# Kernel optimization log

Hardware: AMD Instinct MI355X
Metric: run time of the kernel (lower is better)

The kernel has to match this reference:

```python
import jax, jax.numpy as jnp
import numpy as np

N_USER, N_FOOD, N_ING, N_CAT, N_HAB = 50000, 50000, 50000, 5000, 5000
N_NODES = N_USER + N_FOOD + N_ING + N_CAT + N_HAB  # 160000
E = 600000
R = 8
D = 128  # common_dim == hidden_dim


def _linear(x, W, b):
    # W: (in, out)
    return x @ W + b


def _rgcn_conv(x, src, dst, edge_type, W, root, bias):
    """PyG RGCNConv with aggr='mean': out = x@root + bias + sum_r mean_{r-edges into i}(W_r x_j)."""
    n = x.shape[0]
    out = x @ root + bias
    for r in range(R):  # static small loop over relations
        mask = (edge_type == r)
        h_r = x @ W[r]                          # (N, O)
        msg = h_r[src] * mask[:, None].astype(x.dtype)  # (E, O)
        s = jax.ops.segment_sum(msg, dst, num_segments=n)
        cnt = jax.ops.segment_sum(mask.astype(x.dtype), dst, num_segments=n)
        out = out + s / jnp.maximum(cnt, 1.0)[:, None]
    return out


def setup_inputs() -> dict:
    key = jax.random.key(0)
    ks = jax.random.split(key, 32)
    s = 0.05
    inp = {
        'x_user': jax.random.normal(ks[0], (N_USER, 256), jnp.float32),
        'x_food': jax.random.normal(ks[1], (N_FOOD, 128), jnp.float32),
        'x_ingredient': jax.random.normal(ks[2], (N_ING, 128), jnp.float32),
        'x_category': jax.random.normal(ks[3], (N_CAT, 64), jnp.float32),
        'x_habit': jax.random.normal(ks[4], (N_HAB, 64), jnp.float32),
        'edge_index': jax.random.randint(ks[5], (2, E), 0, N_NODES, jnp.int32),
        'edge_type': jax.random.randint(ks[6], (E,), 0, R, jnp.int32),
        # init linears (in, out)
        'Wu': jax.random.normal(ks[7], (256, D), jnp.float32) * s,
        'bu': jnp.zeros((D,), jnp.float32),
        'Wf': jax.random.normal(ks[8], (128, D), jnp.float32) * s,
        'bf': jnp.zeros((D,), jnp.float32),
        'Wi': jax.random.normal(ks[9], (128, D), jnp.float32) * s,
        'bi': jnp.zeros((D,), jnp.float32),
        'Wc': jax.random.normal(ks[10], (64, D), jnp.float32) * s,
        'bc': jnp.zeros((D,), jnp.float32),
        'Wh': jax.random.normal(ks[11], (64, D), jnp.float32) * s,
        'bh': jnp.zeros((D,), jnp.float32),
        # conv1
        'W1': jax.random.normal(ks[12], (R, D, D), jnp.float32) * s,
        'root1': jax.random.normal(ks[13], (D, D), jnp.float32) * s,
        'bias1': jnp.zeros((D,), jnp.float32),
        # conv2
        'W2': jax.random.normal(ks[14], (R, D, D), jnp.float32) * s,
        'root2': jax.random.normal(ks[15], (D, D), jnp.float32) * s,
        'bias2': jnp.zeros((D,), jnp.float32),
    }
    return inp


def reference(x_user, x_food, x_ingredient, x_category, x_habit,
              edge_index, edge_type,
              Wu, bu, Wf, bf, Wi, bi, Wc, bc, Wh, bh,
              W1, root1, bias1, W2, root2, bias2):
    # per-type input projections then concat in fixed order
    x_all = jnp.concatenate([
        _linear(x_user, Wu, bu),
        _linear(x_food, Wf, bf),
        _linear(x_ingredient, Wi, bi),
        _linear(x_category, Wc, bc),
        _linear(x_habit, Wh, bh),
    ], axis=0)  # (N_NODES, D)
    src, dst = edge_index[0], edge_index[1]
    x = _rgcn_conv(x_all, src, dst, edge_type, W1, root1, bias1)
    x = jax.nn.relu(x)
    # dropout is identity in eval mode
    x = _rgcn_conv(x, src, dst, edge_type, W2, root2, bias2)
    return x
```

## Files before the change

kernel.cpp:

```cpp
#include <hip/hip_runtime.h>

typedef unsigned short ushort_t;
typedef unsigned int uint_t;
typedef __attribute__((ext_vector_type(8))) __bf16 bf16x8;
typedef __attribute__((ext_vector_type(4))) float f32x4;
typedef __attribute__((ext_vector_type(4))) uint_t uint4v;

#define NN 160000
#define DD 128
#define EE 600000
#define RR 8
#define NRR (NN * RR)
#define CAP1 486000
#define WTOT 376832

__device__ __forceinline__ ushort_t f2b(float f) {
  uint_t u = __float_as_uint(f);
  u = u + 0x7fffu + ((u >> 16) & 1u);
  return (ushort_t)(u >> 16);
}
__device__ __forceinline__ float b2f(ushort_t u) {
  return __uint_as_float(((uint_t)u) << 16);
}

struct WSrcs { const float* s[9]; };

__global__ void wconv_all_kernel(WSrcs srcs, ushort_t* __restrict__ wbuf) {
  int i = blockIdx.x * blockDim.x + threadIdx.x;
  if (i >= WTOT) return;
  int m, start, K;
  if      (i < 32768)  { m = 0; start = 0;      K = 256; }
  else if (i < 49152)  { m = 1; start = 32768;  K = 128; }
  else if (i < 65536)  { m = 2; start = 49152;  K = 128; }
  else if (i < 73728)  { m = 3; start = 65536;  K = 64;  }
  else if (i < 81920)  { m = 4; start = 73728;  K = 64;  }
  else if (i < 98304)  { m = 5; start = 81920;  K = 128; }
  else if (i < 114688) { m = 6; start = 98304;  K = 128; }
  else if (i < 245760) { m = 7; start = 114688; K = 128; }
  else                 { m = 8; start = 245760; K = 128; }
  int local = i - start;
  int per = K * 128;
  int mat = local / per, rem = local - mat * per;
  int k = rem >> 7, n = rem & 127;
  wbuf[start + mat * per + n * K + k] = f2b(srcs.s[m][local]);
}

__global__ __launch_bounds__(256, 2) void gemm_proj(
    const float* __restrict__ Ain, const ushort_t* __restrict__ WT,
    const float* __restrict__ bias, ushort_t* __restrict__ Cout, int M, int K) {
  __shared__ ushort_t As[128 * 128];
  __shared__ ushort_t Ws[128 * 128];
  const int tid = threadIdx.x;
  const int bm = blockIdx.x * 128;
  const int wave = tid >> 6, lane = tid & 63;
  const int lr = lane & 15;
  const int lg = lane >> 4;

  f32x4 acc[2][8];
#pragma unroll
  for (int mt = 0; mt < 2; ++mt)
#pragma unroll
    for (int nt = 0; nt < 8; ++nt) acc[mt][nt] = {0.f, 0.f, 0.f, 0.f};

  for (int k0 = 0; k0 < K; k0 += 128) {
#pragma unroll
    for (int it = 0; it < 8; ++it) {
      int row = it * 16 + (tid >> 4);
      int c = tid & 15;
      uint4v val = {0, 0, 0, 0};
      int grow = bm + row, gk = k0 + c * 8;
      if (grow < M && gk < K) {
        const float* ap = Ain + (size_t)grow * K + gk;
        float4 v0 = *(const float4*)ap;
        float4 v1 = *(const float4*)(ap + 4);
        val[0] = (uint_t)f2b(v0.x) | ((uint_t)f2b(v0.y) << 16);
        val[1] = (uint_t)f2b(v0.z) | ((uint_t)f2b(v0.w) << 16);
        val[2] = (uint_t)f2b(v1.x) | ((uint_t)f2b(v1.y) << 16);
        val[3] = (uint_t)f2b(v1.z) | ((uint_t)f2b(v1.w) << 16);
      }
      *(uint4v*)&As[row * 128 + ((c ^ (row & 7)) * 8)] = val;
    }
#pragma unroll
    for (int it = 0; it < 8; ++it) {
      int n = it * 16 + (tid >> 4);
      int c = tid & 15;
      uint4v val = {0, 0, 0, 0};
      int gk = k0 + c * 8;
      if (gk < K)
        val = *(const uint4v*)(WT + (size_t)n * K + gk);
      *(uint4v*)&Ws[n * 128 + ((c ^ (n & 7)) * 8)] = val;
    }
    __syncthreads();
#pragma unroll
    for (int ks = 0; ks < 4; ++ks) {
      int chunk = ks * 4 + lg;
      bf16x8 af[2], bfr[8];
#pragma unroll
      for (int mt = 0; mt < 2; ++mt) {
        int row = wave * 32 + mt * 16 + lr;
        af[mt] = *(const bf16x8*)&As[row * 128 + ((chunk ^ (row & 7)) * 8)];
      }
#pragma unroll
      for (int nt = 0; nt < 8; ++nt) {
        int n = nt * 16 + lr;
        bfr[nt] = *(const bf16x8*)&Ws[n * 128 + ((chunk ^ (n & 7)) * 8)];
      }
#pragma unroll
      for (int mt = 0; mt < 2; ++mt)
#pragma unroll
        for (int nt = 0; nt < 8; ++nt)
          acc[mt][nt] = __builtin_amdgcn_mfma_f32_16x16x32_bf16(
              af[mt], bfr[nt], acc[mt][nt], 0, 0, 0);
    }
    __syncthreads();
  }

  float bv[8];
#pragma unroll
  for (int nt = 0; nt < 8; ++nt) bv[nt] = bias[nt * 16 + lr];

#pragma unroll
  for (int mt = 0; mt < 2; ++mt) {
    int rbase = bm + wave * 32 + mt * 16 + lg * 4;
#pragma unroll
    for (int i = 0; i < 4; ++i) {
      int row = rbase + i;
      if (row >= M) continue;
#pragma unroll
      for (int nt = 0; nt < 8; ++nt)
        Cout[(size_t)row * 128 + nt * 16 + lr] = f2b(acc[mt][nt][i] + bv[nt]);
    }
  }
}

__global__ __launch_bounds__(256, 3) void gemm_rel_agg(
    const ushort_t* __restrict__ xb, const int* __restrict__ segrow,
    const int* __restrict__ sorted_src, const int* __restrict__ rowstart,
    const int* __restrict__ perm,
    const ushort_t* __restrict__ WT_all, ushort_t* __restrict__ tC) {
  __shared__ ushort_t As[64 * 128];
  __shared__ ushort_t Ws[128 * 128];
  const int rel = blockIdx.y;
  const int start = rowstart[rel], end = rowstart[rel + 1];
  const int bm = start + blockIdx.x * 64;
  if (bm >= end) return;
  const ushort_t* WT = WT_all + (size_t)rel * 16384;
  const int tid = threadIdx.x;
  const int wave = tid >> 6, lane = tid & 63;
  const int lr = lane & 15, lg = lane >> 4;
  const int grp = tid >> 4;
  const int sl = tid & 15;

  int gs[4], ge[4];
#pragma unroll
  for (int q = 0; q < 4; ++q) {
    int g = bm + q * 16 + grp;
    bool v = g < end;
    gs[q] = v ? segrow[g] : 0;
    ge[q] = v ? segrow[g + 1] : 0;
  }
  int fs[4];
#pragma unroll
  for (int q = 0; q < 4; ++q)
    fs[q] = (ge[q] > gs[q]) ? sorted_src[gs[q]] : 0;
  uint4v fv[4];
#pragma unroll
  for (int q = 0; q < 4; ++q)
    fv[q] = *(const uint4v*)(xb + (size_t)fs[q] * DD + sl * 8);

#pragma unroll
  for (int q = 0; q < 4; ++q) {
    int row = q * 16 + grp;
    int cnt = ge[q] - gs[q];
    uint4v o = {0, 0, 0, 0};
    if (cnt == 1) {
      o = fv[q];
    } else if (cnt > 1) {
      float a[8];
#pragma unroll
      for (int j = 0; j < 4; ++j) {
        a[j * 2]     = b2f((ushort_t)(fv[q][j] & 0xffff));
        a[j * 2 + 1] = b2f((ushort_t)(fv[q][j] >> 16));
      }
      for (int i = gs[q] + 1; i < ge[q]; ++i) {
        int s = sorted_src[i];
        uint4v v2 = *(const uint4v*)(xb + (size_t)s * DD + sl * 8);
#pragma unroll
        for (int j = 0; j < 4; ++j) {
          a[j * 2]     += b2f((ushort_t)(v2[j] & 0xffff));
          a[j * 2 + 1] += b2f((ushort_t)(v2[j] >> 16));
        }
      }
      float sc = 1.0f / (float)cnt;
#pragma unroll
      for (int j = 0; j < 4; ++j)
        o[j] = (uint_t)f2b(a[j * 2] * sc) | ((uint_t)f2b(a[j * 2 + 1] * sc) << 16);
    }
    *(uint4v*)&As[row * 128 + ((sl ^ (row & 7)) * 8)] = o;
  }
#pragma unroll
  for (int it = 0; it < 8; ++it) {
    int n = it * 16 + grp;
    uint4v val = *(const uint4v*)(WT + (size_t)n * 128 + sl * 8);
    *(uint4v*)&Ws[n * 128 + ((sl ^ (n & 7)) * 8)] = val;
  }
  __syncthreads();

  f32x4 acc[8];
#pragma unroll
  for (int nt = 0; nt < 8; ++nt) acc[nt] = {0.f, 0.f, 0.f, 0.f};

#pragma unroll
  for (int ks = 0; ks < 4; ++ks) {
    int chunk = ks * 4 + lg;
    int arow = wave * 16 + lr;
    bf16x8 af = *(const bf16x8*)&As[arow * 128 + ((chunk ^ (arow & 7)) * 8)];
    bf16x8 bfr[8];
#pragma unroll
    for (int nt = 0; nt < 8; ++nt) {
      int n = nt * 16 + lr;
      bfr[nt] = *(const bf16x8*)&Ws[n * 128 + ((chunk ^ (n & 7)) * 8)];
    }
#pragma unroll
    for (int nt = 0; nt < 8; ++nt)
      acc[nt] = __builtin_amdgcn_mfma_f32_16x16x32_bf16(af, bfr[nt], acc[nt], 0, 0, 0);
  }

  int rbase = bm + wave * 16 + lg * 4;
#pragma unroll
  for (int i = 0; i < 4; ++i) {
    int row = rbase + i;
    if (row >= end) continue;
    int prow = perm[row];
#pragma unroll
    for (int nt = 0; nt < 8; ++nt)
      tC[(size_t)prow * 128 + nt * 16 + lr] = f2b(acc[nt][i]);
  }
}

template <bool RELU_BF>
__global__ __launch_bounds__(256, 3) void gemm_root_combine(
    const ushort_t* __restrict__ Axb, const ushort_t* __restrict__ WT,
    const float* __restrict__ bias, const int* __restrict__ dstrow,
    const ushort_t* __restrict__ tC, float* __restrict__ fout,
    ushort_t* __restrict__ xbout) {
  __shared__ ushort_t smem[24576];
  ushort_t* As = smem;
  ushort_t* Ws = smem + 64 * 128;
  const int tid = threadIdx.x;
  const int bm = blockIdx.x * 64;
  const int wave = tid >> 6, lane = tid & 63;
  const int lr = lane & 15, lg = lane >> 4;
  const int grp = tid >> 4, sl = tid & 15;

#pragma unroll
  for (int it = 0; it < 4; ++it) {
    int row = it * 16 + grp;
    uint4v val = *(const uint4v*)(Axb + (size_t)(bm + row) * 128 + sl * 8);
    *(uint4v*)&As[row * 128 + ((sl ^ (row & 7)) * 8)] = val;
  }
#pragma unroll
  for (int it = 0; it < 8; ++it) {
    int n = it * 16 + grp;
    uint4v val = *(const uint4v*)(WT + (size_t)n * 128 + sl * 8);
    *(uint4v*)&Ws[n * 128 + ((sl ^ (n & 7)) * 8)] = val;
  }
  int wbase = bm + wave * 16;
  int bnd = (lane <= 16) ? dstrow[wbase + lane] : 0;
  __syncthreads();

  f32x4 acc[8];
#pragma unroll
  for (int nt = 0; nt < 8; ++nt) acc[nt] = {0.f, 0.f, 0.f, 0.f};

#pragma unroll
  for (int ks = 0; ks < 4; ++ks) {
    int chunk = ks * 4 + lg;
    int arow = wave * 16 + lr;
    bf16x8 af = *(const bf16x8*)&As[arow * 128 + ((chunk ^ (arow & 7)) * 8)];
    bf16x8 bfr[8];
#pragma unroll
    for (int nt = 0; nt < 8; ++nt) {
      int n = nt * 16 + lr;
      bfr[nt] = *(const bf16x8*)&Ws[n * 128 + ((chunk ^ (n & 7)) * 8)];
    }
#pragma unroll
    for (int nt = 0; nt < 8; ++nt)
      acc[nt] = __builtin_amdgcn_mfma_f32_16x16x32_bf16(af, bfr[nt], acc[nt], 0, 0, 0);
  }
  __syncthreads();

  float* Cs = (float*)smem;
  float bv[8];
#pragma unroll
  for (int nt = 0; nt < 8; ++nt) bv[nt] = bias[nt * 16 + lr];
  {
    int rl0 = wave * 16 + lg * 4;
#pragma unroll
    for (int i = 0; i < 4; ++i)
#pragma unroll
      for (int nt = 0; nt < 8; ++nt)
        Cs[(rl0 + i) * 128 + ((nt * 16 + lr) ^ (lg * 8))] = acc[nt][i] + bv[nt];
  }
  __syncthreads();

  const uint_t* tCu = (const uint_t*)tC;

  for (int rr = 0; rr < 16; ++rr) {
    int rl = wave * 16 + rr;
    int dstn = bm + rl;
    int ps0 = __shfl(bnd, rr), ps1 = __shfl(bnd, rr + 1);
    int k = ps1 - ps0;
    int swzh = ((rr >> 2) & 3) * 4;
    float2 v = ((const float2*)(Cs + (size_t)rl * 128))[lane ^ swzh];
    uint_t tv[8];
#pragma unroll
    for (int j = 0; j < 8; ++j) {
      int idx = ps0 + ((j < k) ? j : 0);
      tv[j] = tCu[(size_t)idx * 64 + lane];
    }
#pragma unroll
    for (int j = 0; j < 8; ++j) {
      uint_t t = (j < k) ? tv[j] : 0u;
      v.x += b2f((ushort_t)(t & 0xffff));
      v.y += b2f((ushort_t)(t >> 16));
    }
    if (RELU_BF) {
      uint_t o = (uint_t)f2b(fmaxf(v.x, 0.f)) | ((uint_t)f2b(fmaxf(v.y, 0.f)) << 16);
      ((uint_t*)(xbout + (size_t)dstn * 128))[lane] = o;
    } else {
      ((float2*)(fout + (size_t)dstn * 128))[lane] = v;
    }
  }
}

__global__ void count_kernel(const int* __restrict__ dstv, const int* __restrict__ et,
                             int* __restrict__ cnt, int E) {
  int e = blockIdx.x * blockDim.x + threadIdx.x;
  if (e < E) atomicAdd(&cnt[(size_t)et[e] * NN + dstv[e]], 1);
}

__global__ __launch_bounds__(256) void scan1_dual(const int* __restrict__ in,
                                                  int* __restrict__ outA, int* __restrict__ outB,
                                                  int* __restrict__ pA, int* __restrict__ pB, int n) {
  __shared__ int sumsA[256], sumsB[256];
  int tid = threadIdx.x;
  int base = blockIdx.x * 2048 + tid * 8;
  int vA[8], vB[8];
  int sA = 0, sB = 0;
#pragma unroll
  for (int i = 0; i < 8; ++i) {
    int idx = base + i;
    int x = (idx < n) ? in[idx] : 0;
    vA[i] = sA; vB[i] = sB;
    sA += x; sB += (x > 0) ? 1 : 0;
  }
  sumsA[tid] = sA; sumsB[tid] = sB;
  __syncthreads();
  for (int off = 1; off < 256; off <<= 1) {
    int tA = (tid >= off) ? sumsA[tid - off] : 0;
    int tB = (tid >= off) ? sumsB[tid - off] : 0;
    __syncthreads();
    sumsA[tid] += tA; sumsB[tid] += tB;
    __syncthreads();
  }
  int exA = (tid == 0) ? 0 : sumsA[tid - 1];
  int exB = (tid == 0) ? 0 : sumsB[tid - 1];
  if (tid == 255) { pA[blockIdx.x] = sumsA[255]; pB[blockIdx.x] = sumsB[255]; }
#pragma unroll
  for (int i = 0; i < 8; ++i) {
    int idx = base + i;
    if (idx < n) { outA[idx] = exA + vA[i]; outB[idx] = exB + vB[i]; }
  }
}

__global__ __launch_bounds__(256) void scan2_two(int* __restrict__ pA, int* __restrict__ pB, int nb) {
  __shared__ int sums[256];
  int* partials = blockIdx.x ? pB : pA;
  int tid = threadIdx.x;
  int per = (nb + 255) / 256;
  int start = tid * per;
  int s = 0;
  for (int i = 0; i < per; ++i) {
    int idx = start + i;
    if (idx < nb) s += partials[idx];
  }
  sums[tid] = s;
  __syncthreads();
  for (int off = 1; off < 256; off <<= 1) {
    int t = (tid >= off) ? sums[tid - off] : 0;
    __syncthreads();
    sums[tid] += t;
    __syncthreads();
  }
  int excl = (tid == 0) ? 0 : sums[tid - 1];
  for (int i = 0; i < per; ++i) {
    int idx = start + i;
    if (idx < nb) {
      int t = partials[idx];
      partials[idx] = excl;
      excl += t;
    }
  }
}

__global__ void scan3_dual(int* __restrict__ outA, int* __restrict__ outB,
                           const int* __restrict__ pA, const int* __restrict__ pB, int n) {
  int base = blockIdx.x * 2048 + threadIdx.x * 8;
  int aA = pA[blockIdx.x], aB = pB[blockIdx.x];
#pragma unroll
  for (int i = 0; i < 8; ++i) {
    int idx = base + i;
    if (idx < n) { outA[idx] += aA; outB[idx] += aB; }
  }
}

__global__ __launch_bounds__(256) void scan1_kernel(const int* __restrict__ in, int* __restrict__ out,
                                                    int* __restrict__ partials, int n) {
  __shared__ int sums[256];
  int tid = threadIdx.x;
  int base = blockIdx.x * 2048 + tid * 8;
  int v[8];
  int s = 0;
#pragma unroll
  for (int i = 0; i < 8; ++i) {
    int idx = base + i;
    int x = (idx < n) ? in[idx] : 0;
    v[i] = s;
    s += x;
  }
  sums[tid] = s;
  __syncthreads();
  for (int off = 1; off < 256; off <<= 1) {
    int t = (tid >= off) ? sums[tid - off] : 0;
    __syncthreads();
    sums[tid] += t;
    __syncthreads();
  }
  int excl = (tid == 0) ? 0 : sums[tid - 1];
  if (tid == 255) partials[blockIdx.x] = sums[255];
#pragma unroll
  for (int i = 0; i < 8; ++i) {
    int idx = base + i;
    if (idx < n) out[idx] = excl + v[i];
  }
}

__global__ __launch_bounds__(256) void scan2_kernel(int* __restrict__ partials, int nb) {
  __shared__ int sums[256];
  int tid = threadIdx.x;
  int per = (nb + 255) / 256;
  int start = tid * per;
  int s = 0;
  for (int i = 0; i < per; ++i) {
    int idx = start + i;
    if (idx < nb) s += partials[idx];
  }
  sums[tid] = s;
  __syncthreads();
  for (int off = 1; off < 256; off <<= 1) {
    int t = (tid >= off) ? sums[tid - off] : 0;
    __syncthreads();
    sums[tid] += t;
    __syncthreads();
  }
  int excl = (tid == 0) ? 0 : sums[tid - 1];
  for (int i = 0; i < per; ++i) {
    int idx = start + i;
    if (idx < nb) {
      int t = partials[idx];
      partials[idx] = excl;
      excl += t;
    }
  }
}

__global__ void scan3_kernel(int* __restrict__ out, const int* __restrict__ partials, int n) {
  int base = blockIdx.x * 2048 + threadIdx.x * 8;
  int add = partials[blockIdx.x];
#pragma unroll
  for (int i = 0; i < 8; ++i) {
    int idx = base + i;
    if (idx < n) out[idx] += add;
  }
}

__global__ void activecnt_kernel(const int* __restrict__ cnt, int* __restrict__ ac) {
  int d = blockIdx.x * blockDim.x + threadIdx.x;
  if (d >= NN) return;
  int s = 0;
#pragma unroll
  for (int r = 0; r < RR; ++r) s += (cnt[(size_t)r * NN + d] > 0) ? 1 : 0;
  ac[d] = s;
}

__global__ void finalize_kernel(const int* __restrict__ cnt, int* __restrict__ seg_off,
                                const int* __restrict__ rowid, int* __restrict__ rowstart,
                                int* __restrict__ segrow, int* __restrict__ dstrow) {
  int t = threadIdx.x;
  if (t == 0) seg_off[NRR] = EE;
  if (t < 8) rowstart[t] = rowid[(size_t)t * NN];
  if (t == 8) {
    int total = rowid[NRR - 1] + (cnt[NRR - 1] > 0 ? 1 : 0);
    rowstart[8] = total;
    segrow[total] = EE;
    dstrow[NN] = total;
  }
}

__global__ void build_kernel(const int* __restrict__ cnt, const int* __restrict__ rowid,
                             const int* __restrict__ seg_off, const int* __restrict__ dstrow,
                             int* __restrict__ segrow, int* __restrict__ perm) {
  int d = blockIdx.x * blockDim.x + threadIdx.x;
  if (d >= NN) return;
  int ds = dstrow[d];
  int rank = 0;
#pragma unroll
  for (int r = 0; r < RR; ++r) {
    size_t p = (size_t)r * NN + d;
    if (cnt[p] > 0) {
      int rw = rowid[p];
      segrow[rw] = seg_off[p];
      perm[rw] = ds + rank;
      ++rank;
    }
  }
}

__global__ void place_kernel(const int* __restrict__ srcv, const int* __restrict__ dstv,
                             const int* __restrict__ et, const int* __restrict__ seg_off,
                             int* __restrict__ cursor, int* __restrict__ sorted_src, int E) {
  int e = blockIdx.x * blockDim.x + threadIdx.x;
  if (e < E) {
    int p = et[e] * NN + dstv[e];
    int slot = seg_off[p] + atomicAdd(&cursor[p], 1);
    sorted_src[slot] = srcv[e];
  }
}

static inline void launch_proj(const float* A, const ushort_t* WT, const float* bias,
                               ushort_t* C, int M, int K, hipStream_t stream) {
  hipLaunchKernelGGL(gemm_proj, dim3((M + 127) / 128), dim3(256), 0, stream,
                     A, WT, bias, C, M, K);
}

extern "C" void kernel_launch(void* const* d_in, const int* in_sizes, int n_in,
                              void* d_out, int out_size, void* d_ws, size_t ws_size,
                              hipStream_t stream) {
  const float* x_user = (const float*)d_in[0];
  const float* x_food = (const float*)d_in[1];
  const float* x_ing  = (const float*)d_in[2];
  const float* x_cat  = (const float*)d_in[3];
  const float* x_hab  = (const float*)d_in[4];
  const int*   eidx   = (const int*)d_in[5];
  const int*   etype  = (const int*)d_in[6];
  const float* Wu = (const float*)d_in[7];
  const float* bu = (const float*)d_in[8];
  const float* Wf = (const float*)d_in[9];
  const float* bfp = (const float*)d_in[10];
  const float* Wi = (const float*)d_in[11];
  const float* bi = (const float*)d_in[12];
  const float* Wc = (const float*)d_in[13];
  const float* bc = (const float*)d_in[14];
  const float* Wh = (const float*)d_in[15];
  const float* bh = (const float*)d_in[16];
  const float* W1    = (const float*)d_in[17];
  const float* root1 = (const float*)d_in[18];
  const float* bias1 = (const float*)d_in[19];
  const float* W2    = (const float*)d_in[20];
  const float* root2 = (const float*)d_in[21];
  const float* bias2 = (const float*)d_in[22];

  const int* src = eidx;
  const int* dst = eidx + EE;

  char* ws = (char*)d_ws;
  ushort_t* xb  = (ushort_t*)(ws);
  ushort_t* tC  = (ushort_t*)(ws + 40960000);
  int* seg_off  = (int*)(ws + 40960000);
  int* rowid    = (int*)(ws + 46080064);
  int* cnt_i    = (int*)(ws + 51200064);
  int* activec  = (int*)(ws + 56320064);
  int* segrow   = (int*)(ws + 165376000);
  int* perm     = (int*)(ws + 167320064);
  int* dstrow   = (int*)(ws + 169264128);
  int* sorted_src = (int*)(ws + 169904192);
  int* rowstart   = (int*)(ws + 172304192);
  int* pA         = (int*)(ws + 172304256);
  int* pB         = (int*)(ws + 172308352);
  ushort_t* wbuf  = (ushort_t*)(ws + 172312448);

  ushort_t* WuT = wbuf;
  ushort_t* WfT = wbuf + 32768;
  ushort_t* WiT = wbuf + 49152;
  ushort_t* WcT = wbuf + 65536;
  ushort_t* WhT = wbuf + 73728;
  ushort_t* r1T = wbuf + 81920;
  ushort_t* r2T = wbuf + 98304;
  ushort_t* W1T = wbuf + 114688;
  ushort_t* W2T = wbuf + 245760;

  float* out = (float*)d_out;

  WSrcs wsrc;
  wsrc.s[0] = Wu; wsrc.s[1] = Wf; wsrc.s[2] = Wi; wsrc.s[3] = Wc; wsrc.s[4] = Wh;
  wsrc.s[5] = root1; wsrc.s[6] = root2; wsrc.s[7] = W1; wsrc.s[8] = W2;
  hipLaunchKernelGGL(wconv_all_kernel, dim3((WTOT + 255) / 256), dim3(256), 0, stream,
                     wsrc, wbuf);

  launch_proj(x_user, WuT, bu, xb + (size_t)0 * DD,      50000, 256, stream);
  launch_proj(x_food, WfT, bfp, xb + (size_t)50000 * DD, 50000, 128, stream);
  launch_proj(x_ing,  WiT, bi, xb + (size_t)100000 * DD, 50000, 128, stream);
  launch_proj(x_cat,  WcT, bc, xb + (size_t)150000 * DD, 5000,  64,  stream);
  launch_proj(x_hab,  WhT, bh, xb + (size_t)155000 * DD, 5000,  64,  stream);

  hipMemsetAsync(cnt_i, 0, (size_t)NRR * 4, stream);
  hipLaunchKernelGGL(count_kernel, dim3((EE + 255) / 256), dim3(256), 0, stream,
                     dst, etype, cnt_i, EE);
  {
    int nb = (NRR + 2047) / 2048;
    hipLaunchKernelGGL(scan1_dual, dim3(nb), dim3(256), 0, stream,
                       cnt_i, seg_off, rowid, pA, pB, NRR);
    hipLaunchKernelGGL(scan2_two, dim3(2), dim3(256), 0, stream, pA, pB, nb);
    hipLaunchKernelGGL(scan3_dual, dim3(nb), dim3(256), 0, stream,
                       seg_off, rowid, pA, pB, NRR);
  }
  hipLaunchKernelGGL(activecnt_kernel, dim3((NN + 255) / 256), dim3(256), 0, stream,
                     cnt_i, activec);
  {
    int nb = (NN + 2047) / 2048;
    hipLaunchKernelGGL(scan1_kernel, dim3(nb), dim3(256), 0, stream, activec, dstrow, pA, NN);
    hipLaunchKernelGGL(scan2_kernel, dim3(1), dim3(256), 0, stream, pA, nb);
    hipLaunchKernelGGL(scan3_kernel, dim3(nb), dim3(256), 0, stream, dstrow, pA, NN);
  }
  hipLaunchKernelGGL(finalize_kernel, dim3(1), dim3(64), 0, stream,
                     cnt_i, seg_off, rowid, rowstart, segrow, dstrow);
  hipLaunchKernelGGL(build_kernel, dim3((NN + 255) / 256), dim3(256), 0, stream,
                     cnt_i, rowid, seg_off, dstrow, segrow, perm);
  hipMemsetAsync(cnt_i, 0, (size_t)NRR * 4, stream);
  hipLaunchKernelGGL(place_kernel, dim3((EE + 255) / 256), dim3(256), 0, stream,
                     src, dst, etype, seg_off, cnt_i, sorted_src, EE);

  const dim3 relGrid(1024, RR);
  const dim3 rootGrid(NN / 64);

  hipLaunchKernelGGL(gemm_rel_agg, relGrid, dim3(256), 0, stream,
                     xb, segrow, sorted_src, rowstart, perm, W1T, tC);
  hipLaunchKernelGGL((gemm_root_combine<true>), rootGrid, dim3(256), 0, stream,
                     xb, r1T, bias1, dstrow, tC, (float*)nullptr, xb);

  hipLaunchKernelGGL(gemm_rel_agg, relGrid, dim3(256), 0, stream,
                     xb, segrow, sorted_src, rowstart, perm, W2T, tC);
  hipLaunchKernelGGL((gemm_root_combine<false>), rootGrid, dim3(256), 0, stream,
                     xb, r2T, bias2, dstrow, tC, out, (ushort_t*)nullptr);
}
```

Measured before the change: 471.4 us.

## Fuse relation aggregation and root GEMM into one per-layer RGCN kernel

Replaces the per-relation compacted GEMM (which wrote transformed rows to a scratch buffer) and the separate root-combine kernel with one kernel per layer. Each 64-row block loops over the root weight and all eight relation weights, aggregating neighbour means into shared memory and accumulating every MFMA result in registers. This removes the large intermediate tC write and read and the compaction preprocessing (dual scan, active counts, perm and dstrow builds). The cost is dense GEMM work over all node-relation pairs, including empty ones, and nine serialized weight loads and barriers per block. A second bf16 buffer is added so the first layer no longer writes its output in place.

```diff
diff --git a/kernel.cpp b/kernel.cpp
--- a/kernel.cpp
+++ b/kernel.cpp
@@ -11,7 +11,6 @@
 #define EE 600000
 #define RR 8
 #define NRR (NN * RR)
-#define CAP1 486000
 #define WTOT 376832
 
 __device__ __forceinline__ ushort_t f2b(float f) {
@@ -133,203 +132,126 @@
   }
 }
 
-__global__ __launch_bounds__(256, 3) void gemm_rel_agg(
-    const ushort_t* __restrict__ xb, const int* __restrict__ segrow,
-    const int* __restrict__ sorted_src, const int* __restrict__ rowstart,
-    const int* __restrict__ perm,
-    const ushort_t* __restrict__ WT_all, ushort_t* __restrict__ tC) {
+template <bool RELU_BF>
+__global__ __launch_bounds__(256, 3) void rgcn_conv(
+    const ushort_t* __restrict__ xin, const int* __restrict__ seg_off,
+    const int* __restrict__ sorted_src,
+    const ushort_t* __restrict__ WrT,
+    const ushort_t* __restrict__ rootT,
+    const float* __restrict__ bias,
+    float* __restrict__ fout, ushort_t* __restrict__ bfout) {
   __shared__ ushort_t As[64 * 128];
   __shared__ ushort_t Ws[128 * 128];
-  const int rel = blockIdx.y;
-  const int start = rowstart[rel], end = rowstart[rel + 1];
-  const int bm = start + blockIdx.x * 64;
-  if (bm >= end) return;
-  const ushort_t* WT = WT_all + (size_t)rel * 16384;
   const int tid = threadIdx.x;
+  const int bm = blockIdx.x * 64;
   const int wave = tid >> 6, lane = tid & 63;
   const int lr = lane & 15, lg = lane >> 4;
   const int grp = tid >> 4;
   const int sl = tid & 15;
 
-  int gs[4], ge[4];
-#pragma unroll
-  for (int q = 0; q < 4; ++q) {
-    int g = bm + q * 16 + grp;
-    bool v = g < end;
-    gs[q] = v ? segrow[g] : 0;
-    ge[q] = v ? segrow[g + 1] : 0;
-  }
-  int fs[4];
-#pragma unroll
-  for (int q = 0; q < 4; ++q)
-    fs[q] = (ge[q] > gs[q]) ? sorted_src[gs[q]] : 0;
-  uint4v fv[4];
-#pragma unroll
-  for (int q = 0; q < 4; ++q)
-    fv[q] = *(const uint4v*)(xb + (size_t)fs[q] * DD + sl * 8);
-
-#pragma unroll
-  for (int q = 0; q < 4; ++q) {
-    int row = q * 16 + grp;
-    int cnt = ge[q] - gs[q];
-    uint4v o = {0, 0, 0, 0};
-    if (cnt == 1) {
-      o = fv[q];
-    } else if (cnt > 1) {
-      float a[8];
-#pragma unroll
-      for (int j = 0; j < 4; ++j) {
-        a[j * 2]     = b2f((ushort_t)(fv[q][j] & 0xffff));
-        a[j * 2 + 1] = b2f((ushort_t)(fv[q][j] >> 16));
-      }
-      for (int i = gs[q] + 1; i < ge[q]; ++i) {
-        int s = sorted_src[i];
-        uint4v v2 = *(const uint4v*)(xb + (size_t)s * DD + sl * 8);
-#pragma unroll
-        for (int j = 0; j < 4; ++j) {
-          a[j * 2]     += b2f((ushort_t)(v2[j] & 0xffff));
-          a[j * 2 + 1] += b2f((ushort_t)(v2[j] >> 16));
+  f32x4 acc[8];
+#pragma unroll
+  for (int nt = 0; nt < 8; ++nt) acc[nt] = {0.f, 0.f, 0.f, 0.f};
+
+  for (int ph = 0; ph < 9; ++ph) {
+    if (ph == 0) {
+#pragma unroll
+      for (int q = 0; q < 4; ++q) {
+        int row = q * 16 + grp;
+        uint4v val = *(const uint4v*)(xin + (size_t)(bm + row) * DD + sl * 8);
+        *(uint4v*)&As[row * 128 + ((sl ^ (row & 7)) * 8)] = val;
+      }
+    } else {
+      const int rel = ph - 1;
+      int gs[4], ge[4];
+#pragma unroll
+      for (int q = 0; q < 4; ++q) {
+        const int* sp = seg_off + (size_t)rel * NN + (bm + q * 16 + grp);
+        gs[q] = sp[0];
+        ge[q] = sp[1];
+      }
+      int fs[4];
+#pragma unroll
+      for (int q = 0; q < 4; ++q)
+        fs[q] = (ge[q] > gs[q]) ? sorted_src[gs[q]] : 0;
+      uint4v fv[4];
+#pragma unroll
+      for (int q = 0; q < 4; ++q)
+        fv[q] = *(const uint4v*)(xin + (size_t)fs[q] * DD + sl * 8);
+
+#pragma unroll
+      for (int q = 0; q < 4; ++q) {
+        int row = q * 16 + grp;
+        int cnt = ge[q] - gs[q];
+        uint4v o = {0, 0, 0, 0};
+        if (cnt == 1) {
+          o = fv[q];
+        } else if (cnt > 1) {
+          float a[8];
+#pragma unroll
+          for (int j = 0; j < 4; ++j) {
+            a[j * 2]     = b2f((ushort_t)(fv[q][j] & 0xffff));
+            a[j * 2 + 1] = b2f((ushort_t)(fv[q][j] >> 16));
+          }
+          for (int i = gs[q] + 1; i < ge[q]; ++i) {
+            int s = sorted_src[i];
+            uint4v v2 = *(const uint4v*)(xin + (size_t)s * DD + sl * 8);
+#pragma unroll
+            for (int j = 0; j < 4; ++j) {
+              a[j * 2]     += b2f((ushort_t)(v2[j] & 0xffff));
+              a[j * 2 + 1] += b2f((ushort_t)(v2[j] >> 16));
+            }
+          }
+          float sc = 1.0f / (float)cnt;
+#pragma unroll
+          for (int j = 0; j < 4; ++j)
+            o[j] = (uint_t)f2b(a[j * 2] * sc) | ((uint_t)f2b(a[j * 2 + 1] * sc) << 16);
         }
-      }
-      float sc = 1.0f / (float)cnt;
-#pragma unroll
-      for (int j = 0; j < 4; ++j)
-        o[j] = (uint_t)f2b(a[j * 2] * sc) | ((uint_t)f2b(a[j * 2 + 1] * sc) << 16);
-    }
-    *(uint4v*)&As[row * 128 + ((sl ^ (row & 7)) * 8)] = o;
-  }
-#pragma unroll
-  for (int it = 0; it < 8; ++it) {
-    int n = it * 16 + grp;
-    uint4v val = *(const uint4v*)(WT + (size_t)n * 128 + sl * 8);
-    *(uint4v*)&Ws[n * 128 + ((sl ^ (n & 7)) * 8)] = val;
-  }
-  __syncthreads();
-
-  f32x4 acc[8];
-#pragma unroll
-  for (int nt = 0; nt < 8; ++nt) acc[nt] = {0.f, 0.f, 0.f, 0.f};
-
-#pragma unroll
-  for (int ks = 0; ks < 4; ++ks) {
-    int chunk = ks * 4 + lg;
-    int arow = wave * 16 + lr;
-    bf16x8 af = *(const bf16x8*)&As[arow * 128 + ((chunk ^ (arow & 7)) * 8)];
-    bf16x8 bfr[8];
-#pragma unroll
-    for (int nt = 0; nt < 8; ++nt) {
-      int n = nt * 16 + lr;
-      bfr[nt] = *(const bf16x8*)&Ws[n * 128 + ((chunk ^ (n & 7)) * 8)];
-    }
-#pragma unroll
-    for (int nt = 0; nt < 8; ++nt)
-      acc[nt] = __builtin_amdgcn_mfma_f32_16x16x32_bf16(af, bfr[nt], acc[nt], 0, 0, 0);
-  }
+        *(uint4v*)&As[row * 128 + ((sl ^ (row & 7)) * 8)] = o;
+      }
+    }
+    const ushort_t* WT = (ph == 0) ? rootT : (WrT + (size_t)(ph - 1) * 16384);
+#pragma unroll
+    for (int it = 0; it < 8; ++it) {
+      int n = it * 16 + grp;
+      uint4v val = *(const uint4v*)(WT + (size_t)n * 128 + sl * 8);
+      *(uint4v*)&Ws[n * 128 + ((sl ^ (n & 7)) * 8)] = val;
+    }
+    __syncthreads();
+
+#pragma unroll
+    for (int ks = 0; ks < 4; ++ks) {
+      int chunk = ks * 4 + lg;
+      int arow = wave * 16 + lr;
+      bf16x8 af = *(const bf16x8*)&As[arow * 128 + ((chunk ^ (arow & 7)) * 8)];
+      bf16x8 bfr[8];
+#pragma unroll
+      for (int nt = 0; nt < 8; ++nt) {
+        int n = nt * 16 + lr;
+        bfr[nt] = *(const bf16x8*)&Ws[n * 128 + ((chunk ^ (n & 7)) * 8)];
+      }
+#pragma unroll
+      for (int nt = 0; nt < 8; ++nt)
+        acc[nt] = __builtin_amdgcn_mfma_f32_16x16x32_bf16(af, bfr[nt], acc[nt], 0, 0, 0);
+    }
+    __syncthreads();
+  }
+
+  float bv[8];
+#pragma unroll
+  for (int nt = 0; nt < 8; ++nt) bv[nt] = bias[nt * 16 + lr];
 
   int rbase = bm + wave * 16 + lg * 4;
 #pragma unroll
   for (int i = 0; i < 4; ++i) {
     int row = rbase + i;
-    if (row >= end) continue;
-    int prow = perm[row];
-#pragma unroll
-    for (int nt = 0; nt < 8; ++nt)
-      tC[(size_t)prow * 128 + nt * 16 + lr] = f2b(acc[nt][i]);
-  }
-}
-
-template <bool RELU_BF>
-__global__ __launch_bounds__(256, 3) void gemm_root_combine(
-    const ushort_t* __restrict__ Axb, const ushort_t* __restrict__ WT,
-    const float* __restrict__ bias, const int* __restrict__ dstrow,
-    const ushort_t* __restrict__ tC, float* __restrict__ fout,
-    ushort_t* __restrict__ xbout) {
-  __shared__ ushort_t smem[24576];
-  ushort_t* As = smem;
-  ushort_t* Ws = smem + 64 * 128;
-  const int tid = threadIdx.x;
-  const int bm = blockIdx.x * 64;
-  const int wave = tid >> 6, lane = tid & 63;
-  const int lr = lane & 15, lg = lane >> 4;
-  const int grp = tid >> 4, sl = tid & 15;
-
-#pragma unroll
-  for (int it = 0; it < 4; ++it) {
-    int row = it * 16 + grp;
-    uint4v val = *(const uint4v*)(Axb + (size_t)(bm + row) * 128 + sl * 8);
-    *(uint4v*)&As[row * 128 + ((sl ^ (row & 7)) * 8)] = val;
-  }
-#pragma unroll
-  for (int it = 0; it < 8; ++it) {
-    int n = it * 16 + grp;
-    uint4v val = *(const uint4v*)(WT + (size_t)n * 128 + sl * 8);
-    *(uint4v*)&Ws[n * 128 + ((sl ^ (n & 7)) * 8)] = val;
-  }
-  int wbase = bm + wave * 16;
-  int bnd = (lane <= 16) ? dstrow[wbase + lane] : 0;
-  __syncthreads();
-
-  f32x4 acc[8];
-#pragma unroll
-  for (int nt = 0; nt < 8; ++nt) acc[nt] = {0.f, 0.f, 0.f, 0.f};
-
-#pragma unroll
-  for (int ks = 0; ks < 4; ++ks) {
-    int chunk = ks * 4 + lg;
-    int arow = wave * 16 + lr;
-    bf16x8 af = *(const bf16x8*)&As[arow * 128 + ((chunk ^ (arow & 7)) * 8)];
-    bf16x8 bfr[8];
 #pragma unroll
     for (int nt = 0; nt < 8; ++nt) {
-      int n = nt * 16 + lr;
-      bfr[nt] = *(const bf16x8*)&Ws[n * 128 + ((chunk ^ (n & 7)) * 8)];
-    }
-#pragma unroll
-    for (int nt = 0; nt < 8; ++nt)
-      acc[nt] = __builtin_amdgcn_mfma_f32_16x16x32_bf16(af, bfr[nt], acc[nt], 0, 0, 0);
-  }
-  __syncthreads();
-
-  float* Cs = (float*)smem;
-  float bv[8];
-#pragma unroll
-  for (int nt = 0; nt < 8; ++nt) bv[nt] = bias[nt * 16 + lr];
-  {
-    int rl0 = wave * 16 + lg * 4;
-#pragma unroll
-    for (int i = 0; i < 4; ++i)
-#pragma unroll
-      for (int nt = 0; nt < 8; ++nt)
-        Cs[(rl0 + i) * 128 + ((nt * 16 + lr) ^ (lg * 8))] = acc[nt][i] + bv[nt];
-  }
-  __syncthreads();
-
-  const uint_t* tCu = (const uint_t*)tC;
-
-  for (int rr = 0; rr < 16; ++rr) {
-    int rl = wave * 16 + rr;
-    int dstn = bm + rl;
-    int ps0 = __shfl(bnd, rr), ps1 = __shfl(bnd, rr + 1);
-    int k = ps1 - ps0;
-    int swzh = ((rr >> 2) & 3) * 4;
-    float2 v = ((const float2*)(Cs + (size_t)rl * 128))[lane ^ swzh];
-    uint_t tv[8];
-#pragma unroll
-    for (int j = 0; j < 8; ++j) {
-      int idx = ps0 + ((j < k) ? j : 0);
-      tv[j] = tCu[(size_t)idx * 64 + lane];
-    }
-#pragma unroll
-    for (int j = 0; j < 8; ++j) {
-      uint_t t = (j < k) ? tv[j] : 0u;
-      v.x += b2f((ushort_t)(t & 0xffff));
-      v.y += b2f((ushort_t)(t >> 16));
-    }
-    if (RELU_BF) {
-      uint_t o = (uint_t)f2b(fmaxf(v.x, 0.f)) | ((uint_t)f2b(fmaxf(v.y, 0.f)) << 16);
-      ((uint_t*)(xbout + (size_t)dstn * 128))[lane] = o;
-    } else {
-      ((float2*)(fout + (size_t)dstn * 128))[lane] = v;
+      float v = acc[nt][i] + bv[nt];
+      if (RELU_BF)
+        bfout[(size_t)row * 128 + nt * 16 + lr] = f2b(fmaxf(v, 0.f));
+      else
+        fout[(size_t)row * 128 + nt * 16 + lr] = v;
     }
   }
 }
@@ -338,81 +260,6 @@
                              int* __restrict__ cnt, int E) {
   int e = blockIdx.x * blockDim.x + threadIdx.x;
   if (e < E) atomicAdd(&cnt[(size_t)et[e] * NN + dstv[e]], 1);
-}
-
-__global__ __launch_bounds__(256) void scan1_dual(const int* __restrict__ in,
-                                                  int* __restrict__ outA, int* __restrict__ outB,
-                                                  int* __restrict__ pA, int* __restrict__ pB, int n) {
-  __shared__ int sumsA[256], sumsB[256];
-  int tid = threadIdx.x;
-  int base = blockIdx.x * 2048 + tid * 8;
-  int vA[8], vB[8];
-  int sA = 0, sB = 0;
-#pragma unroll
-  for (int i = 0; i < 8; ++i) {
-    int idx = base + i;
-    int x = (idx < n) ? in[idx] : 0;
-    vA[i] = sA; vB[i] = sB;
-    sA += x; sB += (x > 0) ? 1 : 0;
-  }
-  sumsA[tid] = sA; sumsB[tid] = sB;
-  __syncthreads();
-  for (int off = 1; off < 256; off <<= 1) {
-    int tA = (tid >= off) ? sumsA[tid - off] : 0;
-    int tB = (tid >= off) ? sumsB[tid - off] : 0;
-    __syncthreads();
-    sumsA[tid] += tA; sumsB[tid] += tB;
-    __syncthreads();
-  }
-  int exA = (tid == 0) ? 0 : sumsA[tid - 1];
-  int exB = (tid == 0) ? 0 : sumsB[tid - 1];
-  if (tid == 255) { pA[blockIdx.x] = sumsA[255]; pB[blockIdx.x] = sumsB[255]; }
-#pragma unroll
-  for (int i = 0; i < 8; ++i) {
-    int idx = base + i;
-    if (idx < n) { outA[idx] = exA + vA[i]; outB[idx] = exB + vB[i]; }
-  }
-}
-
-__global__ __launch_bounds__(256) void scan2_two(int* __restrict__ pA, int* __restrict__ pB, int nb) {
-  __shared__ int sums[256];
-  int* partials = blockIdx.x ? pB : pA;
-  int tid = threadIdx.x;
-  int per = (nb + 255) / 256;
-  int start = tid * per;
-  int s = 0;
-  for (int i = 0; i < per; ++i) {
-    int idx = start + i;
-    if (idx < nb) s += partials[idx];
-  }
-  sums[tid] = s;
-  __syncthreads();
-  for (int off = 1; off < 256; off <<= 1) {
-    int t = (tid >= off) ? sums[tid - off] : 0;
-    __syncthreads();
-    sums[tid] += t;
-    __syncthreads();
-  }
-  int excl = (tid == 0) ? 0 : sums[tid - 1];
-  for (int i = 0; i < per; ++i) {
-    int idx = start + i;
-    if (idx < nb) {
-      int t = partials[idx];
-      partials[idx] = excl;
-      excl += t;
-    }
-  }
-}
-
-__global__ void scan3_dual(int* __restrict__ outA, int* __restrict__ outB,
-                           const int* __restrict__ pA, const int* __restrict__ pB, int n) {
-  int base = blockIdx.x * 2048 + threadIdx.x * 8;
-  int aA = pA[blockIdx.x], aB = pB[blockIdx.x];
-#pragma unroll
-  for (int i = 0; i < 8; ++i) {
-    int idx = base + i;
-    if (idx < n) { outA[idx] += aA; outB[idx] += aB; }
-  }
 }
 
 __global__ __launch_bounds__(256) void scan1_kernel(const int* __restrict__ in, int* __restrict__ out,
@@ -485,46 +332,8 @@
   }
 }
 
-__global__ void activecnt_kernel(const int* __restrict__ cnt, int* __restrict__ ac) {
-  int d = blockIdx.x * blockDim.x + threadIdx.x;
-  if (d >= NN) return;
-  int s = 0;
-#pragma unroll
-  for (int r = 0; r < RR; ++r) s += (cnt[(size_t)r * NN + d] > 0) ? 1 : 0;
-  ac[d] = s;
-}
-
-__global__ void finalize_kernel(const int* __restrict__ cnt, int* __restrict__ seg_off,
-                                const int* __restrict__ rowid, int* __restrict__ rowstart,
-                                int* __restrict__ segrow, int* __restrict__ dstrow) {
-  int t = threadIdx.x;
-  if (t == 0) seg_off[NRR] = EE;
-  if (t < 8) rowstart[t] = rowid[(size_t)t * NN];
-  if (t == 8) {
-    int total = rowid[NRR - 1] + (cnt[NRR - 1] > 0 ? 1 : 0);
-    rowstart[8] = total;
-    segrow[total] = EE;
-    dstrow[NN] = total;
-  }
-}
-
-__global__ void build_kernel(const int* __restrict__ cnt, const int* __restrict__ rowid,
-                             const int* __restrict__ seg_off, const int* __restrict__ dstrow,
-                             int* __restrict__ segrow, int* __restrict__ perm) {
-  int d = blockIdx.x * blockDim.x + threadIdx.x;
-  if (d >= NN) return;
-  int ds = dstrow[d];
-  int rank = 0;
-#pragma unroll
-  for (int r = 0; r < RR; ++r) {
-    size_t p = (size_t)r * NN + d;
-    if (cnt[p] > 0) {
-      int rw = rowid[p];
-      segrow[rw] = seg_off[p];
-      perm[rw] = ds + rank;
-      ++rank;
-    }
-  }
+__global__ void sentinel_kernel(int* __restrict__ seg_off) {
+  seg_off[NRR] = EE;
 }
 
 __global__ void place_kernel(const int* __restrict__ srcv, const int* __restrict__ dstv,
@@ -575,20 +384,13 @@
   const int* dst = eidx + EE;
 
   char* ws = (char*)d_ws;
-  ushort_t* xb  = (ushort_t*)(ws);
-  ushort_t* tC  = (ushort_t*)(ws + 40960000);
-  int* seg_off  = (int*)(ws + 40960000);
-  int* rowid    = (int*)(ws + 46080064);
-  int* cnt_i    = (int*)(ws + 51200064);
-  int* activec  = (int*)(ws + 56320064);
-  int* segrow   = (int*)(ws + 165376000);
-  int* perm     = (int*)(ws + 167320064);
-  int* dstrow   = (int*)(ws + 169264128);
-  int* sorted_src = (int*)(ws + 169904192);
-  int* rowstart   = (int*)(ws + 172304192);
-  int* pA         = (int*)(ws + 172304256);
-  int* pB         = (int*)(ws + 172308352);
-  ushort_t* wbuf  = (ushort_t*)(ws + 172312448);
+  ushort_t* xb   = (ushort_t*)(ws);
+  ushort_t* xb2  = (ushort_t*)(ws + 40960000);
+  int* seg_off   = (int*)(ws + 81920000);
+  int* cnt_i     = (int*)(ws + 87040064);
+  int* sorted_src= (int*)(ws + 92160064);
+  int* pA        = (int*)(ws + 94560064);
+  ushort_t* wbuf = (ushort_t*)(ws + 94564160);
 
   ushort_t* WuT = wbuf;
   ushort_t* WfT = wbuf + 32768;
@@ -619,38 +421,20 @@
                      dst, etype, cnt_i, EE);
   {
     int nb = (NRR + 2047) / 2048;
-    hipLaunchKernelGGL(scan1_dual, dim3(nb), dim3(256), 0, stream,
-                       cnt_i, seg_off, rowid, pA, pB, NRR);
-    hipLaunchKernelGGL(scan2_two, dim3(2), dim3(256), 0, stream, pA, pB, nb);
-    hipLaunchKernelGGL(scan3_dual, dim3(nb), dim3(256), 0, stream,
-                       seg_off, rowid, pA, pB, NRR);
-  }
-  hipLaunchKernelGGL(activecnt_kernel, dim3((NN + 255) / 256), dim3(256), 0, stream,
-                     cnt_i, activec);
-  {
-    int nb = (NN + 2047) / 2048;
-    hipLaunchKernelGGL(scan1_kernel, dim3(nb), dim3(256), 0, stream, activec, dstrow, pA, NN);
+    hipLaunchKernelGGL(scan1_kernel, dim3(nb), dim3(256), 0, stream, cnt_i, seg_off, pA, NRR);
     hipLaunchKernelGGL(scan2_kernel, dim3(1), dim3(256), 0, stream, pA, nb);
-    hipLaunchKernelGGL(scan3_kernel, dim3(nb), dim3(256), 0, stream, dstrow, pA, NN);
-  }
-  hipLaunchKernelGGL(finalize_kernel, dim3(1), dim3(64), 0, stream,
-                     cnt_i, seg_off, rowid, rowstart, segrow, dstrow);
-  hipLaunchKernelGGL(build_kernel, dim3((NN + 255) / 256), dim3(256), 0, stream,
-                     cnt_i, rowid, seg_off, dstrow, segrow, perm);
+    hipLaunchKernelGGL(scan3_kernel, dim3(nb), dim3(256), 0, stream, seg_off, pA, NRR);
+  }
+  hipLaunchKernelGGL(sentinel_kernel, dim3(1), dim3(1), 0, stream, seg_off);
   hipMemsetAsync(cnt_i, 0, (size_t)NRR * 4, stream);
   hipLaunchKernelGGL(place_kernel, dim3((EE + 255) / 256), dim3(256), 0, stream,
                      src, dst, etype, seg_off, cnt_i, sorted_src, EE);
 
-  const dim3 relGrid(1024, RR);
-  const dim3 rootGrid(NN / 64);
-
-  hipLaunchKernelGGL(gemm_rel_agg, relGrid, dim3(256), 0, stream,
-                     xb, segrow, sorted_src, rowstart, perm, W1T, tC);
-  hipLaunchKernelGGL((gemm_root_combine<true>), rootGrid, dim3(256), 0, stream,
-                     xb, r1T, bias1, dstrow, tC, (float*)nullptr, xb);
-
-  hipLaunchKernelGGL(gemm_rel_agg, relGrid, dim3(256), 0, stream,
-                     xb, segrow, sorted_src, rowstart, perm, W2T, tC);
-  hipLaunchKernelGGL((gemm_root_combine<false>), rootGrid, dim3(256), 0, stream,
-                     xb, r2T, bias2, dstrow, tC, out, (ushort_t*)nullptr);
-}
+  const dim3 convGrid(NN / 64);
+
+  hipLaunchKernelGGL((rgcn_conv<true>), convGrid, dim3(256), 0, stream,
+                     xb, seg_off, sorted_src, W1T, r1T, bias1, (float*)nullptr, xb2);
+
+  hipLaunchKernelGGL((rgcn_conv<false>), convGrid, dim3(256), 0, stream,
+                     xb2, seg_off, sorted_src, W2T, r2T, bias2, out, (ushort_t*)nullptr);
+}
```

Result: no change. 479.5 us (+1.7%).
